# Kernel optimization log

Measured on AMD Instinct MI355X. Metric: run time of the kernel, lower is better.

## Reference

```python
import jax, jax.numpy as jnp
import numpy as np

DIM = 1024
NUM_HEADS = 16
HEAD_DIM = DIM // NUM_HEADS
SCALE = HEAD_DIM ** -0.5


def apply_rope(x):
    # x: [B, H, S, D]; rotate pairs (x1, x2) split as first/second half of D
    S, D = x.shape[-2], x.shape[-1]
    pos = jnp.arange(S, dtype=jnp.float32)[:, None]                      # [S, 1]
    freqs = jnp.exp(jnp.arange(0, D, 2, dtype=jnp.float32) * (-np.log(10000.0) / D))  # [D/2]
    emb = pos * freqs                                                    # [S, D/2]
    cos = jnp.cos(emb)[None, None, :, :].astype(x.dtype)                 # [1,1,S,D/2]
    sin = jnp.sin(emb)[None, None, :, :].astype(x.dtype)
    x1, x2 = jnp.split(x, 2, axis=-1)
    return jnp.concatenate([x1 * cos - x2 * sin, x1 * sin + x2 * cos], axis=-1)


def setup_inputs() -> dict:
    key = jax.random.key(0)
    ks = jax.random.split(key, 6)
    B, S = 2, 2048
    x = jax.random.normal(ks[0], (B, S, DIM), dtype=jnp.float32)
    # torch nn.Linear weights: [out_features, in_features]
    w_std = DIM ** -0.5
    wq = jax.random.normal(ks[1], (DIM, DIM), dtype=jnp.float32) * w_std
    wk = jax.random.normal(ks[2], (DIM, DIM), dtype=jnp.float32) * w_std
    wv = jax.random.normal(ks[3], (DIM, DIM), dtype=jnp.float32) * w_std
    wo = jax.random.normal(ks[4], (DIM, DIM), dtype=jnp.float32) * w_std
    wo_b = jax.random.normal(ks[5], (DIM,), dtype=jnp.float32) * 0.01
    return {"x": x, "wq": wq, "wk": wk, "wv": wv, "wo": wo, "wo_b": wo_b}


def reference(x, wq, wk, wv, wo, wo_b):
    B, S, _ = x.shape
    def proj(w):
        # y = x @ w.T -> [B, S, dim] -> [B, H, S, head_dim]
        y = jnp.einsum('bsd,ed->bse', x, w)
        return y.reshape(B, S, NUM_HEADS, HEAD_DIM).transpose(0, 2, 1, 3)
    q = apply_rope(proj(wq))
    k = apply_rope(proj(wk))
    v = proj(wv)
    attn = jnp.einsum('bhqd,bhkd->bhqk', q, k) * SCALE   # [B,H,S,S]
    attn = jax.nn.softmax(attn, axis=-1)                 # dropout is identity in eval
    out = jnp.einsum('bhqk,bhkd->bhqd', attn, v)         # [B,H,S,D]
    out = out.transpose(0, 2, 1, 3).reshape(B, S, DIM)
    return jnp.einsum('bsd,ed->bse', out, wo) + wo_b
```

## Files before the change

### kernel.cpp

```cpp
#include <hip/hip_runtime.h>
#include <hip/hip_bf16.h>

typedef __attribute__((ext_vector_type(8))) short s16x8;
typedef __attribute__((ext_vector_type(4))) short s16x4;
typedef __attribute__((ext_vector_type(4))) float f32x4;

#define SEQ 2048
#define NB 2
#define NH 16
#define HD 64
#define DIM 1024
#define MR (NB * SEQ)
#define NT (SEQ / 64)
#define QSC 0.18033688011112042f

__device__ __forceinline__ unsigned short f2b(float f) {
    unsigned u = __float_as_uint(f);
    u += 0x7fffu + ((u >> 16) & 1u);
    return (unsigned short)(u >> 16);
}

__device__ __forceinline__ unsigned pk2(float a, float b) {
    unsigned r;
    asm("v_cvt_pk_bf16_f32 %0, %1, %2" : "=v"(r) : "v"(a), "v"(b));
    return r;
}

__device__ __forceinline__ s16x8 mk8(unsigned a, unsigned b, unsigned c, unsigned d) {
    union { unsigned u[4]; s16x8 v; } x;
    x.u[0] = a; x.u[1] = b; x.u[2] = c; x.u[3] = d;
    return x.v;
}

__device__ __forceinline__ s16x8 cat8(s16x4 a, s16x4 b) {
    union { s16x4 h[2]; s16x8 v; } x;
    x.h[0] = a; x.h[1] = b;
    return x.v;
}

__device__ __forceinline__ void gl_lds16(const unsigned short* g, unsigned short* l) {
    __builtin_amdgcn_global_load_lds(
        (const __attribute__((address_space(1))) void*)g,
        (__attribute__((address_space(3))) void*)l, 16, 0, 0);
}

__device__ __forceinline__ unsigned ldsoff(const void* p) {
    return (unsigned)(size_t)(const __attribute__((address_space(3))) void*)p;
}

__device__ __forceinline__ void cast4(const float* __restrict__ src, unsigned short* __restrict__ dst, int i) {
    float4 v = reinterpret_cast<const float4*>(src)[i];
    ushort4 o;
    o.x = f2b(v.x); o.y = f2b(v.y); o.z = f2b(v.z); o.w = f2b(v.w);
    reinterpret_cast<ushort4*>(dst)[i] = o;
}

__global__ __launch_bounds__(256) void prep_kernel(
    const float* __restrict__ x, const float* __restrict__ wq, const float* __restrict__ wk,
    const float* __restrict__ wv, const float* __restrict__ wo,
    unsigned short* __restrict__ xb, unsigned short* __restrict__ wqkv,
    unsigned short* __restrict__ wwo, float2* __restrict__ tab)
{
    int b = blockIdx.x, t = threadIdx.x;
    if (b < 4096)       cast4(x,  xb,                 b * 256 + t);
    else if (b < 5120)  cast4(wq, wqkv,               (b - 4096) * 256 + t);
    else if (b < 6144)  cast4(wk, wqkv + DIM * DIM,   (b - 5120) * 256 + t);
    else if (b < 7168)  cast4(wv, wqkv + 2 * DIM * DIM, (b - 6144) * 256 + t);
    else if (b < 8192)  cast4(wo, wwo,                (b - 7168) * 256 + t);
    else {
        int i = (b - 8192) * 256 + t;
        int pos = i >> 5, fi = i & 31;
        float freq = expf((float)fi * (-9.210340371976184f / 32.0f));
        float emb = (float)pos * freq;
        tab[i] = make_float2(cosf(emb), sinf(emb));
    }
}

template <int EPI>
__global__ __launch_bounds__(64, 2) void gemm_async(
    const unsigned short* __restrict__ A,
    const unsigned short* __restrict__ Bw,
    const float2* __restrict__ tab,
    unsigned short* __restrict__ qw,
    unsigned short* __restrict__ kw,
    unsigned short* __restrict__ vw,
    float* __restrict__ out,
    const float* __restrict__ bias)
{
    __shared__ unsigned short As[2 * 2048];
    __shared__ unsigned short Bs[2 * 4096];
    const int lane = threadIdx.x & 63;
    const int lo = lane & 15, hi = lane >> 4;
    const int wg = blockIdx.x;
    const int xcd = wg & 7, bi = wg >> 3;
    const int bx = bi >> 3;
    const int by = xcd * 8 + (bi & 7);
    const int m0 = by * 64, n0 = bx * 128;

    const unsigned short* agp = A + (long)(m0 + (lane >> 2)) * DIM + (lane & 3) * 8;
    const unsigned short* bgp = Bw + (long)(n0 + (lane >> 2)) * DIM + (lane & 3) * 8;

    f32x4 acc[4][8] = {};

#define STG(buf, k0) {                                       \
        unsigned short* al = &As[(buf) * 2048];              \
        unsigned short* bl = &Bs[(buf) * 4096];              \
        _Pragma("unroll") for (int s = 0; s < 4; ++s)        \
            gl_lds16(agp + (k0) + (long)s * 16 * DIM, al + s * 512); \
        _Pragma("unroll") for (int s = 0; s < 8; ++s)        \
            gl_lds16(bgp + (k0) + (long)s * 16 * DIM, bl + s * 512); }

    STG(0, 0)
    STG(1, 32)

    for (int kt = 0; kt < 32; ++kt) {
        const int cb = kt & 1;
        if (kt < 31) { asm volatile("s_waitcnt vmcnt(12)" ::: "memory"); }
        else         { asm volatile("s_waitcnt vmcnt(0)" ::: "memory"); }
        __builtin_amdgcn_sched_barrier(0);
        s16x8 af[4], bf[8];
#pragma unroll
        for (int i = 0; i < 4; ++i)
            af[i] = *reinterpret_cast<const s16x8*>(&As[cb * 2048 + (i * 16 + lo) * 32 + hi * 8]);
#pragma unroll
        for (int j = 0; j < 8; ++j)
            bf[j] = *reinterpret_cast<const s16x8*>(&Bs[cb * 4096 + (j * 16 + lo) * 32 + hi * 8]);
        asm volatile("s_waitcnt lgkmcnt(0)" ::: "memory");
        __builtin_amdgcn_sched_barrier(0);
        if (kt + 2 < 32) STG(cb, (kt + 2) * 32)
        __builtin_amdgcn_sched_barrier(0);
        __builtin_amdgcn_s_setprio(1);
#pragma unroll
        for (int i = 0; i < 4; ++i)
#pragma unroll
            for (int j = 0; j < 8; ++j)
                acc[i][j] = __builtin_amdgcn_mfma_f32_16x16x32_bf16(af[i], bf[j], acc[i][j], 0, 0, 0);
        __builtin_amdgcn_s_setprio(0);
    }
#undef STG

    if (EPI == 0) {
#pragma unroll
        for (int ai = 0; ai < 4; ++ai) {
#pragma unroll
            for (int g = 0; g < 2; ++g) {
#pragma unroll
                for (int cp = 0; cp < 2; ++cp) {
                    f32x4 v1 = acc[ai][g * 4 + cp];
                    f32x4 v2 = acc[ai][g * 4 + cp + 2];
                    int e = n0 + g * 64 + cp * 16 + lo;
                    int which = e >> 10;
                    int eh = e & 1023;
                    int h = eh >> 6, d = eh & 63;
                    unsigned short* dst = (which == 0) ? qw : ((which == 1) ? kw : vw);
                    float qs = (which == 0) ? QSC : 1.0f;
#pragma unroll
                    for (int r = 0; r < 4; ++r) {
                        int m = m0 + ai * 16 + hi * 4 + r;
                        int b = m >> 11, pos = m & (SEQ - 1);
                        long off = (((long)(b * NH + h)) * SEQ + pos) * HD;
                        if (which == 2) {
                            dst[off + d]      = f2b(v1[r]);
                            dst[off + d + 32] = f2b(v2[r]);
                        } else {
                            float2 cs = tab[pos * 32 + d];
                            dst[off + d]      = f2b((v1[r] * cs.x - v2[r] * cs.y) * qs);
                            dst[off + d + 32] = f2b((v1[r] * cs.y + v2[r] * cs.x) * qs);
                        }
                    }
                }
            }
        }
    } else {
#pragma unroll
        for (int ai = 0; ai < 4; ++ai)
#pragma unroll
            for (int bj = 0; bj < 8; ++bj) {
                int n = n0 + bj * 16 + lo;
                float bv = bias[n];
#pragma unroll
                for (int r = 0; r < 4; ++r) {
                    int m = m0 + ai * 16 + hi * 4 + r;
                    out[(long)m * DIM + n] = acc[ai][bj][r] + bv;
                }
            }
    }
}

__global__ __launch_bounds__(256) void flash_attn(
    const unsigned short* __restrict__ qw,
    const unsigned short* __restrict__ kw,
    const unsigned short* __restrict__ vw,
    unsigned short* __restrict__ ao)
{
    __shared__ __align__(16) unsigned char smem[33792];
    const int t = threadIdx.x;
    const int w = t >> 6, lane = t & 63;
    const int lo = lane & 15, hi = lane >> 4;
    const int wg = blockIdx.x;
    const int swz = (wg & 7) * 128 + (wg >> 3);
    const int bh = swz >> 5;
    const int q0 = (swz & 31) * 64;
    const unsigned short* qh = qw + (long)bh * SEQ * HD;
    const unsigned short* kh = kw + (long)bh * SEQ * HD;
    const unsigned short* vh = vw + (long)bh * SEQ * HD;

    s16x8 qf[4][2];
#pragma unroll
    for (int qt = 0; qt < 4; ++qt)
#pragma unroll
        for (int ds = 0; ds < 2; ++ds)
            qf[qt][ds] = *reinterpret_cast<const s16x8*>(
                qh + (long)(q0 + qt * 16 + lo) * HD + ds * 32 + hi * 8);
    asm volatile("s_waitcnt vmcnt(0)" ::: "memory");

    unsigned char* wbase = smem + w * 8192;
    const int kr0 = lane >> 3, ks0 = (lane & 7) ^ (kr0 & 7);
    const int kr1 = 8 + (lane >> 3), ks1 = (lane & 7) ^ (kr1 & 7);
    const unsigned short* ksrc0 = kh + (16 * w + kr0) * HD + ks0 * 8;
    const unsigned short* ksrc1 = kh + (16 * w + kr1) * HD + ks1 * 8;
    const int c0 = lane, c1 = 64 + lane;
    const int kl0 = ((c0 >> 3 >> 2) << 2) | ((c0 >> 1) & 3);
    const int dd0 = (((c0 >> 3) & 3) << 4) | ((c0 & 1) << 3);
    const int kl1 = ((c1 >> 3 >> 2) << 2) | ((c1 >> 1) & 3);
    const int dd1 = (((c1 >> 3) & 3) << 4) | ((c1 & 1) << 3);
    const unsigned short* vsrc0 = vh + (16 * w + kl0) * HD + dd0;
    const unsigned short* vsrc1 = vh + (16 * w + kl1) * HD + dd1;

#define STAGE(buf, kb) {                                              \
        unsigned short* d_ = (unsigned short*)(wbase + (buf) * 4096); \
        gl_lds16(ksrc0 + (kb) * HD, d_);                              \
        gl_lds16(ksrc1 + (kb) * HD, d_ + 512);                        \
        gl_lds16(vsrc0 + (kb) * HD, d_ + 1024);                       \
        gl_lds16(vsrc1 + (kb) * HD, d_ + 1536); }

    const int kro0 = lo * 128 + ((hi ^ (lo & 7)) << 4);
    const int kro1 = lo * 128 + (((4 + hi) ^ (lo & 7)) << 4);
    const unsigned vtb0 = ldsoff(wbase) + 2048 + hi * 512 + lo * 8;

    f32x4 od[4][4] = {};
    f32x4 lr = {0.f, 0.f, 0.f, 0.f};

    STAGE(0, 0)
    STAGE(1, 64)

    constexpr int NT2 = NT / 2;
    for (int i2 = 0; i2 < NT2; ++i2) {
        const bool more = (i2 + 1 < NT2);
        asm volatile("s_waitcnt vmcnt(4)" ::: "memory");
        s16x8 kf0 = *reinterpret_cast<const s16x8*>(wbase + kro0);
        s16x8 kf1 = *reinterpret_cast<const s16x8*>(wbase + kro1);
        s16x4 va0, va1, va2, va3;
        asm volatile("ds_read_b64_tr_b16 %0, %1"            : "=v"(va0) : "v"(vtb0));
        asm volatile("ds_read_b64_tr_b16 %0, %1 offset:128" : "=v"(va1) : "v"(vtb0));
        asm volatile("ds_read_b64_tr_b16 %0, %1 offset:256" : "=v"(va2) : "v"(vtb0));
        asm volatile("ds_read_b64_tr_b16 %0, %1 offset:384" : "=v"(va3) : "v"(vtb0));
        asm volatile("s_waitcnt lgkmcnt(0)" ::: "memory");
        __builtin_amdgcn_sched_barrier(0);

        f32x4 sc[4] = {};
        __builtin_amdgcn_s_setprio(1);
#pragma unroll
        for (int qt = 0; qt < 4; ++qt)
            sc[qt] = __builtin_amdgcn_mfma_f32_16x16x32_bf16(kf0, qf[qt][0], sc[qt], 0, 0, 0);
#pragma unroll
        for (int qt = 0; qt < 4; ++qt)
            sc[qt] = __builtin_amdgcn_mfma_f32_16x16x32_bf16(kf1, qf[qt][1], sc[qt], 0, 0, 0);
        __builtin_amdgcn_s_setprio(0);
        if (more) STAGE(0, (2 * i2 + 2) * 64)

        unsigned u01[4], u23[4];
#pragma unroll
        for (int qt = 0; qt < 4; ++qt) {
            float p0 = exp2f(sc[qt][0]), p1 = exp2f(sc[qt][1]);
            float p2 = exp2f(sc[qt][2]), p3 = exp2f(sc[qt][3]);
            lr[qt] += (p0 + p1) + (p2 + p3);
            u01[qt] = pk2(p0, p1); u23[qt] = pk2(p2, p3);
        }

        if (more) { asm volatile("s_waitcnt vmcnt(4)" ::: "memory"); }
        else      { asm volatile("s_waitcnt vmcnt(0)" ::: "memory"); }
        s16x8 kg0 = *reinterpret_cast<const s16x8*>(wbase + 4096 + kro0);
        s16x8 kg1 = *reinterpret_cast<const s16x8*>(wbase + 4096 + kro1);
        s16x4 vb0, vb1, vb2, vb3;
        const unsigned vtb1 = vtb0 + 4096;
        asm volatile("ds_read_b64_tr_b16 %0, %1"            : "=v"(vb0) : "v"(vtb1));
        asm volatile("ds_read_b64_tr_b16 %0, %1 offset:128" : "=v"(vb1) : "v"(vtb1));
        asm volatile("ds_read_b64_tr_b16 %0, %1 offset:256" : "=v"(vb2) : "v"(vtb1));
        asm volatile("ds_read_b64_tr_b16 %0, %1 offset:384" : "=v"(vb3) : "v"(vtb1));
        asm volatile("s_waitcnt lgkmcnt(0)" ::: "memory");
        __builtin_amdgcn_sched_barrier(0);

        f32x4 sd[4] = {};
        __builtin_amdgcn_s_setprio(1);
#pragma unroll
        for (int qt = 0; qt < 4; ++qt)
            sd[qt] = __builtin_amdgcn_mfma_f32_16x16x32_bf16(kg0, qf[qt][0], sd[qt], 0, 0, 0);
#pragma unroll
        for (int qt = 0; qt < 4; ++qt)
            sd[qt] = __builtin_amdgcn_mfma_f32_16x16x32_bf16(kg1, qf[qt][1], sd[qt], 0, 0, 0);
        __builtin_amdgcn_s_setprio(0);
        if (more) STAGE(1, (2 * i2 + 3) * 64)

        s16x8 pf8[4];
#pragma unroll
        for (int qt = 0; qt < 4; ++qt) {
            float p0 = exp2f(sd[qt][0]), p1 = exp2f(sd[qt][1]);
            float p2 = exp2f(sd[qt][2]), p3 = exp2f(sd[qt][3]);
            lr[qt] += (p0 + p1) + (p2 + p3);
            pf8[qt] = mk8(u01[qt], u23[qt], pk2(p0, p1), pk2(p2, p3));
        }
        s16x8 vf80 = cat8(va0, vb0), vf81 = cat8(va1, vb1);
        s16x8 vf82 = cat8(va2, vb2), vf83 = cat8(va3, vb3);

        __builtin_amdgcn_s_setprio(1);
#pragma unroll
        for (int qt = 0; qt < 4; ++qt) {
            od[0][qt] = __builtin_amdgcn_mfma_f32_16x16x32_bf16(vf80, pf8[qt], od[0][qt], 0, 0, 0);
            od[1][qt] = __builtin_amdgcn_mfma_f32_16x16x32_bf16(vf81, pf8[qt], od[1][qt], 0, 0, 0);
            od[2][qt] = __builtin_amdgcn_mfma_f32_16x16x32_bf16(vf82, pf8[qt], od[2][qt], 0, 0, 0);
            od[3][qt] = __builtin_amdgcn_mfma_f32_16x16x32_bf16(vf83, pf8[qt], od[3][qt], 0, 0, 0);
        }
        __builtin_amdgcn_s_setprio(0);
    }
#undef STAGE

#pragma unroll
    for (int qt = 0; qt < 4; ++qt) {
        lr[qt] += __shfl_xor(lr[qt], 16);
        lr[qt] += __shfl_xor(lr[qt], 32);
    }
    __syncthreads();
    float* red = reinterpret_cast<float*>(smem);
    float* ldl = reinterpret_cast<float*>(smem + 32768);
    if (lane < 16) {
#pragma unroll
        for (int qt = 0; qt < 4; ++qt) ldl[w * 64 + qt * 16 + lane] = lr[qt];
    }

    const int b = bh >> 4, h = bh & 15;
    const int ql = w * 16 + (lane >> 2);
    const int qc = ql & 7;
    float linv = 0.f;
#pragma unroll
    for (int p = 0; p < 2; ++p) {
        if (p) __syncthreads();
#pragma unroll
        for (int dtp = 0; dtp < 2; ++dtp) {
#pragma unroll
            for (int qt = 0; qt < 4; ++qt) {
                int q = qt * 16 + lo;
                int quad = ((dtp << 2) + hi) ^ (lo & 7);
                *reinterpret_cast<f32x4*>(red + w * 2048 + q * 32 + quad * 4) = od[p * 2 + dtp][qt];
            }
        }
        __syncthreads();
        float s0[8] = {0.f, 0.f, 0.f, 0.f, 0.f, 0.f, 0.f, 0.f};
#pragma unroll
        for (int w2 = 0; w2 < 4; ++w2)
#pragma unroll
            for (int k = 0; k < 2; ++k) {
                int quad = (((lane & 3) << 1) + k) ^ qc;
                f32x4 v = *reinterpret_cast<const f32x4*>(red + w2 * 2048 + ql * 32 + quad * 4);
#pragma unroll
                for (int j = 0; j < 4; ++j) s0[k * 4 + j] += v[j];
            }
        if (p == 0)
            linv = 1.f / (ldl[ql] + ldl[64 + ql] + ldl[128 + ql] + ldl[192 + ql]);
        unsigned uu[4];
#pragma unroll
        for (int k2 = 0; k2 < 4; ++k2)
            uu[k2] = pk2(s0[2 * k2] * linv, s0[2 * k2 + 1] * linv);
        int4 ov;
        ov.x = uu[0]; ov.y = uu[1]; ov.z = uu[2]; ov.w = uu[3];
        *reinterpret_cast<int4*>(ao + ((long)(b * SEQ + q0 + ql)) * DIM +
                                 h * 64 + p * 32 + (lane & 3) * 8) = ov;
    }
}

extern "C" void kernel_launch(void* const* d_in, const int* in_sizes, int n_in,
                              void* d_out, int out_size, void* d_ws, size_t ws_size,
                              hipStream_t stream) {
    const float* x   = (const float*)d_in[0];
    const float* wq  = (const float*)d_in[1];
    const float* wk  = (const float*)d_in[2];
    const float* wv  = (const float*)d_in[3];
    const float* wo  = (const float*)d_in[4];
    const float* wob = (const float*)d_in[5];

    char* ws = (char*)d_ws;
    unsigned short* xb   = (unsigned short*)(ws);
    unsigned short* wqkv = (unsigned short*)(ws + 8388608);
    unsigned short* wwo  = (unsigned short*)(ws + 14680064);
    unsigned short* qw   = (unsigned short*)(ws + 16777216);
    unsigned short* kw   = (unsigned short*)(ws + 25165824);
    unsigned short* vw   = (unsigned short*)(ws + 33554432);
    unsigned short* ao   = (unsigned short*)(ws + 41943040);
    float2* tab          = (float2*)(ws + 50331648);

    prep_kernel<<<8448, 256, 0, stream>>>(x, wq, wk, wv, wo, xb, wqkv, wwo, tab);

    gemm_async<0><<<1536, 64, 0, stream>>>(xb, wqkv, tab, qw, kw, vw, nullptr, nullptr);
    flash_attn<<<1024, 256, 0, stream>>>(qw, kw, vw, ao);
    gemm_async<1><<<512, 64, 0, stream>>>(ao, wwo, nullptr, nullptr, nullptr, nullptr,
                                          (float*)d_out, wob);
}
```

Baseline: 141.5 us.

## Replace QKV projection GEMM with 4-wave 128x128 tiled kernel

Adds a new 256-thread GEMM kernel that computes 128x128 output tiles with four waves, each owning a 64x64 sub-tile. It double-buffers A and B through LDS using async global-to-LDS loads and maps workgroups so each XCD gets a contiguous band of M tiles. The QKV projection launch switches from the single-wave kernel to this one, keeping the fused RoPE, scaling and head-layout epilogue. The larger tile raises data reuse per LDS load and cuts the grid in half, at the cost of more barriers, higher register pressure and lower occupancy per CU.

Result: faster. 127.2 us, median of 2 (-10.1%).

```diff
diff --git a/kernel.cpp b/kernel.cpp
--- a/kernel.cpp
+++ b/kernel.cpp
@@ -73,6 +73,122 @@
         float freq = expf((float)fi * (-9.210340371976184f / 32.0f));
         float emb = (float)pos * freq;
         tab[i] = make_float2(cosf(emb), sinf(emb));
+    }
+}
+
+template <int EPI>
+__global__ __launch_bounds__(256) void gemm_mw(
+    const unsigned short* __restrict__ A,
+    const unsigned short* __restrict__ Bw,
+    const float2* __restrict__ tab,
+    unsigned short* __restrict__ qw,
+    unsigned short* __restrict__ kw,
+    unsigned short* __restrict__ vw,
+    float* __restrict__ out,
+    const float* __restrict__ bias)
+{
+    __shared__ unsigned short As[2][4096];
+    __shared__ unsigned short Bs[2][4096];
+    const int t = threadIdx.x;
+    const int wid = t >> 6, lane = t & 63;
+    const int wr = wid >> 1, wc = wid & 1;
+    const int lo = lane & 15, hi = lane >> 4;
+    const int wg = blockIdx.x;
+    const int xcd = wg & 7, bi = wg >> 3;
+    const int by = xcd * 4 + (bi & 3);
+    const int bx = bi >> 2;
+    const int m0 = by * 128, n0 = bx * 128;
+
+    const unsigned short* agp = A + (long)(m0 + (t >> 2)) * DIM + (t & 3) * 8;
+    const unsigned short* bgp = Bw + (long)(n0 + (t >> 2)) * DIM + (t & 3) * 8;
+    unsigned short* alds = &As[0][0] + wid * 512;
+    unsigned short* blds = &Bs[0][0] + wid * 512;
+
+#define STG(buf, k0) {                                        \
+        gl_lds16(agp + (k0), alds + (buf) * 4096);            \
+        gl_lds16(agp + (k0) + 64 * DIM, alds + (buf) * 4096 + 2048); \
+        gl_lds16(bgp + (k0), blds + (buf) * 4096);            \
+        gl_lds16(bgp + (k0) + 64 * DIM, blds + (buf) * 4096 + 2048); }
+
+    f32x4 acc[4][4] = {};
+    STG(0, 0)
+    STG(1, 32)
+
+    for (int kt = 0; kt < 32; ++kt) {
+        const int cb = kt & 1;
+        if (kt < 31) { asm volatile("s_waitcnt vmcnt(4)" ::: "memory"); }
+        else         { asm volatile("s_waitcnt vmcnt(0)" ::: "memory"); }
+        __builtin_amdgcn_sched_barrier(0);
+        __builtin_amdgcn_s_barrier();
+        __builtin_amdgcn_sched_barrier(0);
+        s16x8 af[4], bf[4];
+#pragma unroll
+        for (int i = 0; i < 4; ++i)
+            af[i] = *reinterpret_cast<const s16x8*>(&As[cb][(wr * 64 + i * 16 + lo) * 32 + hi * 8]);
+#pragma unroll
+        for (int j = 0; j < 4; ++j)
+            bf[j] = *reinterpret_cast<const s16x8*>(&Bs[cb][(wc * 64 + j * 16 + lo) * 32 + hi * 8]);
+        asm volatile("s_waitcnt lgkmcnt(0)" ::: "memory");
+        __builtin_amdgcn_sched_barrier(0);
+        if (kt + 2 < 32) {
+            __builtin_amdgcn_s_barrier();
+            __builtin_amdgcn_sched_barrier(0);
+            STG(cb, (kt + 2) * 32)
+        }
+        __builtin_amdgcn_s_setprio(1);
+#pragma unroll
+        for (int i = 0; i < 4; ++i)
+#pragma unroll
+            for (int j = 0; j < 4; ++j)
+                acc[i][j] = __builtin_amdgcn_mfma_f32_16x16x32_bf16(af[i], bf[j], acc[i][j], 0, 0, 0);
+        __builtin_amdgcn_s_setprio(0);
+    }
+#undef STG
+
+    const int rowb = m0 + wr * 64;
+    const int colb = n0 + wc * 64;
+    if (EPI == 0) {
+#pragma unroll
+        for (int ai = 0; ai < 4; ++ai) {
+#pragma unroll
+            for (int cp = 0; cp < 2; ++cp) {
+                f32x4 v1 = acc[ai][cp];
+                f32x4 v2 = acc[ai][cp + 2];
+                int e = colb + cp * 16 + lo;
+                int which = e >> 10;
+                int eh = e & 1023;
+                int h = eh >> 6, d = eh & 63;
+                unsigned short* dst = (which == 0) ? qw : ((which == 1) ? kw : vw);
+                float qs = (which == 0) ? QSC : 1.0f;
+#pragma unroll
+                for (int r = 0; r < 4; ++r) {
+                    int m = rowb + ai * 16 + hi * 4 + r;
+                    int b = m >> 11, pos = m & (SEQ - 1);
+                    long off = (((long)(b * NH + h)) * SEQ + pos) * HD;
+                    if (which == 2) {
+                        dst[off + d]      = f2b(v1[r]);
+                        dst[off + d + 32] = f2b(v2[r]);
+                    } else {
+                        float2 cs = tab[pos * 32 + d];
+                        dst[off + d]      = f2b((v1[r] * cs.x - v2[r] * cs.y) * qs);
+                        dst[off + d + 32] = f2b((v1[r] * cs.y + v2[r] * cs.x) * qs);
+                    }
+                }
+            }
+        }
+    } else {
+#pragma unroll
+        for (int ai = 0; ai < 4; ++ai)
+#pragma unroll
+            for (int cj = 0; cj < 4; ++cj) {
+                int n = colb + cj * 16 + lo;
+                float bv = bias[n];
+#pragma unroll
+                for (int r = 0; r < 4; ++r) {
+                    int m = rowb + ai * 16 + hi * 4 + r;
+                    out[(long)m * DIM + n] = acc[ai][cj][r] + bv;
+                }
+            }
     }
 }
 
@@ -400,7 +516,7 @@
 
     prep_kernel<<<8448, 256, 0, stream>>>(x, wq, wk, wv, wo, xb, wqkv, wwo, tab);
 
-    gemm_async<0><<<1536, 64, 0, stream>>>(xb, wqkv, tab, qw, kw, vw, nullptr, nullptr);
+    gemm_mw<0><<<768, 256, 0, stream>>>(xb, wqkv, tab, qw, kw, vw, nullptr, nullptr);
     flash_attn<<<1024, 256, 0, stream>>>(qw, kw, vw, ao);
     gemm_async<1><<<512, 64, 0, stream>>>(ao, wwo, nullptr, nullptr, nullptr, nullptr,
                                           (float*)d_out, wob);
```
